# Performance work log

Hardware: AMD Instinct MI355X
Metric: run time of the kernel (lower is better)

Reference implementation:

```python
import jax, jax.numpy as jnp
import numpy as np

N_NODES = 50000
N_EDGES = 800000


def _norm(deg):
    # DGL: norm = deg^-0.5 with inf (zero-degree) replaced by 0
    return jnp.where(deg > 0, jax.lax.rsqrt(jnp.maximum(deg, 1.0)), 0.0)


def setup_inputs() -> dict:
    key = jax.random.key(0)
    ks = jax.random.split(key, 8)
    x = jax.random.normal(ks[0], (N_NODES, 128), dtype=jnp.float32)
    W1 = jax.random.normal(ks[1], (128, 128), dtype=jnp.float32) * (1.0 / np.sqrt(128))
    b1 = jnp.zeros((128,), dtype=jnp.float32)
    W2 = jax.random.normal(ks[2], (128, 8), dtype=jnp.float32) * (1.0 / np.sqrt(128))
    b2 = jnp.zeros((8,), dtype=jnp.float32)
    src = jax.random.randint(ks[3], (N_EDGES,), 0, N_NODES, dtype=jnp.int32)
    dst = jax.random.randint(ks[4], (N_EDGES,), 0, N_NODES, dtype=jnp.int32)
    graph_ids = jnp.sort(jax.random.randint(ks[5], (N_NODES,), 0, 100, dtype=jnp.int32))
    return {"x": x, "W1": W1, "b1": b1, "W2": W2, "b2": b2,
            "src": src, "dst": dst, "graph_ids": graph_ids, "num_graphs": 100}


def _graph_conv(x, W, b, src, dst, norm_src, norm_dst):
    # GraphConv norm='both': out = D_in^{-1/2} A (D_out^{-1/2} x W) + b
    h = x @ W                                   # [N, F_out]
    msg = h[src] * norm_src[src, None]          # gather + src norm, [E, F_out]
    agg = jax.ops.segment_sum(msg, dst, num_segments=x.shape[0])  # scatter-add
    return agg * norm_dst[:, None] + b


def reference(x, W1, b1, W2, b2, src, dst, graph_ids, num_graphs):
    n = x.shape[0]
    ones_e = jnp.ones((src.shape[0],), dtype=x.dtype)
    deg_out = jax.ops.segment_sum(ones_e, src, num_segments=n)
    deg_in = jax.ops.segment_sum(ones_e, dst, num_segments=n)
    norm_src = _norm(deg_out)
    norm_dst = _norm(deg_in)

    h = _graph_conv(x, W1, b1, src, dst, norm_src, norm_dst)
    h = jax.nn.relu(h)
    h = _graph_conv(h, W2, b2, src, dst, norm_src, norm_dst)

    # dgl.mean_nodes: per-graph mean of node features
    counts = jax.ops.segment_sum(jnp.ones((n,), dtype=x.dtype), graph_ids,
                                 num_segments=num_graphs)
    sums = jax.ops.segment_sum(h, graph_ids, num_segments=num_graphs)
    return sums / jnp.maximum(counts, 1.0)[:, None]
```

## Files before the change

### kernel.cpp

```cpp
#include <hip/hip_runtime.h>

#define F1 128
#define F2 8
#define CAP 64
#define RH 8192
#define ECH 16384

typedef unsigned short us8 __attribute__((ext_vector_type(8)));
typedef short b16x8 __attribute__((ext_vector_type(8)));
typedef float f32x4 __attribute__((ext_vector_type(4)));

__device__ inline unsigned short f2bf(float f) {
  unsigned u = __float_as_uint(f);
  u += 0x7FFF + ((u >> 16) & 1);
  return (unsigned short)(u >> 16);
}
__device__ inline float bf2f(unsigned short h) {
  return __uint_as_float(((unsigned)h) << 16);
}

__global__ __launch_bounds__(256) void k_hist(const int* __restrict__ src,
                                              const int* __restrict__ dst,
                                              unsigned short* __restrict__ src16,
                                              unsigned short* __restrict__ dst16,
                                              int* __restrict__ partialA,
                                              int* __restrict__ partialB,
                                              int Epad, int E, int N) {
  __shared__ int binsA[RH];
  __shared__ int binsB[RH];
  int range0 = blockIdx.x * RH;
  int c = blockIdx.y;
  int t = threadIdx.x;
  bool writer = (blockIdx.x == 0);
  for (int i = t; i < RH; i += 256) { binsA[i] = 0; binsB[i] = 0; }
  __syncthreads();
  int e0 = c * ECH, e1 = min(e0 + ECH, Epad);
  for (int base = e0 + t * 4; base < e1; base += 1024) {
    int4 a, b;
    if (base + 4 <= E) {
      a = *(const int4*)&src[base];
      b = *(const int4*)&dst[base];
    } else {
      a.x = (base + 0 < E) ? src[base + 0] : -1;
      a.y = (base + 1 < E) ? src[base + 1] : -1;
      a.z = (base + 2 < E) ? src[base + 2] : -1;
      a.w = (base + 3 < E) ? src[base + 3] : -1;
      b.x = (base + 0 < E) ? dst[base + 0] : -1;
      b.y = (base + 1 < E) ? dst[base + 1] : -1;
      b.z = (base + 2 < E) ? dst[base + 2] : -1;
      b.w = (base + 3 < E) ? dst[base + 3] : -1;
    }
    int av[4] = {a.x, a.y, a.z, a.w};
    int bv[4] = {b.x, b.y, b.z, b.w};
#pragma unroll
    for (int j = 0; j < 4; ++j) {
      int sn = av[j] - range0;
      if (av[j] >= 0 && (unsigned)sn < (unsigned)RH) atomicAdd(&binsA[sn], 1);
      int dn = bv[j] - range0;
      if (bv[j] >= 0 && (unsigned)dn < (unsigned)RH) atomicAdd(&binsB[dn], 1);
    }
    if (writer) {
      ushort4 sa, sb;
      sa.x = av[0] >= 0 ? (unsigned short)av[0] : 0xFFFF;
      sa.y = av[1] >= 0 ? (unsigned short)av[1] : 0xFFFF;
      sa.z = av[2] >= 0 ? (unsigned short)av[2] : 0xFFFF;
      sa.w = av[3] >= 0 ? (unsigned short)av[3] : 0xFFFF;
      sb.x = bv[0] >= 0 ? (unsigned short)bv[0] : 0xFFFF;
      sb.y = bv[1] >= 0 ? (unsigned short)bv[1] : 0xFFFF;
      sb.z = bv[2] >= 0 ? (unsigned short)bv[2] : 0xFFFF;
      sb.w = bv[3] >= 0 ? (unsigned short)bv[3] : 0xFFFF;
      *(ushort4*)&src16[base] = sa;
      *(ushort4*)&dst16[base] = sb;
    }
  }
  __syncthreads();
  for (int i = t; i < RH; i += 256) {
    int n = range0 + i;
    if (n < N) {
      partialA[c * N + n] = binsA[i];
      partialB[c * N + n] = binsB[i];
    }
  }
}

__global__ void k_starts(const int* __restrict__ partialA, const int* __restrict__ partialB,
                         int* __restrict__ starts, int* __restrict__ cnt,
                         float* __restrict__ norm_src, float* __restrict__ norm_dst,
                         unsigned short* __restrict__ esrc16,
                         unsigned short* __restrict__ h1n,
                         float* __restrict__ h2n,
                         float* __restrict__ out,
                         const int* __restrict__ gids,
                         float* __restrict__ rcnt,
                         const float* __restrict__ W1,
                         unsigned short* __restrict__ Wth,
                         unsigned short* __restrict__ Wtl,
                         int N, int NCH, int NG) {
  int n = blockIdx.x * 256 + threadIdx.x;
  if (n < NG * F2) out[n] = 0.f;
  if (n < NG) {
    int g = n;
    int lo = 0, hi = N;
    while (lo < hi) { int m = (lo + hi) >> 1; if (gids[m] < g) lo = m + 1; else hi = m; }
    int lb = lo;
    lo = 0; hi = N;
    while (lo < hi) { int m = (lo + hi) >> 1; if (gids[m] <= g) lo = m + 1; else hi = m; }
    rcnt[g] = 1.f / fmaxf((float)(lo - lb), 1.f);
  }
  if (n < F1 * F1) {
    int k = n >> 7, cc = n & 127;
    float v = W1[n];
    unsigned short hi = f2bf(v);
    unsigned short lo = f2bf(v - bf2f(hi));
    Wth[cc * 128 + k] = hi;
    Wtl[cc * 128 + k] = lo;
  }
  if (n < 16) {
    us8 z = {0, 0, 0, 0, 0, 0, 0, 0};
    *(us8*)&h1n[(size_t)N * 128 + n * 8] = z;
  }
  if (n < 8) h2n[(size_t)N * 8 + n] = 0.f;
  if (n < N) {
    int dout = 0;
#pragma unroll 8
    for (int c = 0; c < NCH; ++c) dout += partialA[c * N + n];
    int run = n * CAP;
#pragma unroll 8
    for (int c = 0; c < NCH; ++c) {
      starts[c * N + n] = run;
      run += partialB[c * N + n];
    }
    int din = run - n * CAP;
    int cn = min(din, CAP);
    cnt[n] = cn;
    int cp = (cn + 15) & ~15;
    for (int pos = cn; pos < cp; ++pos) esrc16[n * CAP + pos] = (unsigned short)N;
    norm_src[n] = dout > 0 ? rsqrtf((float)dout) : 0.f;
    norm_dst[n] = din > 0 ? rsqrtf((float)din) : 0.f;
  }
}

__global__ __launch_bounds__(256) void k_scatter(const unsigned short* __restrict__ src16,
                                                 const unsigned short* __restrict__ dst16,
                                                 const int* __restrict__ starts,
                                                 unsigned short* __restrict__ esrc16,
                                                 int Epad, int N, int NCH) {
  __shared__ int cur[RH];
  int range0 = ((int)blockIdx.x / NCH) * RH;
  int c = (int)blockIdx.x % NCH;
  int t = threadIdx.x;
  for (int i = t; i < RH; i += 256) {
    int n = range0 + i;
    cur[i] = (n < N) ? starts[c * N + n] : 0;
  }
  __syncthreads();
  int e0 = c * ECH, e1 = min(e0 + ECH, Epad);
  for (int base = e0 + t * 8; base < e1; base += 2048) {
    us8 a = *(const us8*)&src16[base];
    us8 b = *(const us8*)&dst16[base];
#pragma unroll
    for (int j = 0; j < 8; ++j) {
      int dn = (int)b[j] - range0;
      if ((unsigned)dn < (unsigned)RH) {
        int node = range0 + dn;
        int p = atomicAdd(&cur[dn], 1);
        if (p < (node + 1) * CAP) esrc16[p] = a[j];
      }
    }
  }
}

__global__ __launch_bounds__(256) void k_gemm1(const float* __restrict__ x,
                                               const unsigned short* __restrict__ Wth,
                                               const unsigned short* __restrict__ Wtl,
                                               const float* __restrict__ norm_src,
                                               unsigned short* __restrict__ h1n, int N) {
  __shared__ unsigned short xh[64][72], xl[64][72];
  __shared__ unsigned short wh[128][72], wl[128][72];
  int tid = threadIdx.x;
  int row0 = blockIdx.x * 64;
  int L = tid & 63;
  int wave = tid >> 6;
  int q = L >> 4, mloc = L & 15;
  int m0 = wave * 16;
  f32x4 acc[8];
#pragma unroll
  for (int t = 0; t < 8; ++t) acc[t] = (f32x4){0.f, 0.f, 0.f, 0.f};

  for (int kb = 0; kb < 2; ++kb) {
    __syncthreads();
#pragma unroll
    for (int it = 0; it < 4; ++it) {
      int flat = tid + it * 256;
      int n = flat >> 3, kg = (flat & 7) * 8;
      us8 vh = *(const us8*)&Wth[n * 128 + kb * 64 + kg];
      us8 vl = *(const us8*)&Wtl[n * 128 + kb * 64 + kg];
      *(us8*)&wh[n][kg] = vh;
      *(us8*)&wl[n][kg] = vl;
    }
#pragma unroll
    for (int it = 0; it < 4; ++it) {
      int idx = tid + it * 256;
      int r = idx >> 4, kk = (idx & 15) * 4;
      int grow = row0 + r;
      float4 v = make_float4(0.f, 0.f, 0.f, 0.f);
      if (grow < N) v = *(const float4*)&x[(size_t)grow * 128 + kb * 64 + kk];
      ushort4 h, l;
      h.x = f2bf(v.x); l.x = f2bf(v.x - bf2f(h.x));
      h.y = f2bf(v.y); l.y = f2bf(v.y - bf2f(h.y));
      h.z = f2bf(v.z); l.z = f2bf(v.z - bf2f(h.z));
      h.w = f2bf(v.w); l.w = f2bf(v.w - bf2f(h.w));
      *(ushort4*)&xh[r][kk] = h;
      *(ushort4*)&xl[r][kk] = l;
    }
    __syncthreads();
#pragma unroll
    for (int ks = 0; ks < 2; ++ks) {
      int koff = ks * 32 + q * 8;
      b16x8 ah = *(const b16x8*)&xh[m0 + mloc][koff];
      b16x8 al = *(const b16x8*)&xl[m0 + mloc][koff];
#pragma unroll
      for (int t = 0; t < 8; ++t) {
        b16x8 bh = *(const b16x8*)&wh[t * 16 + mloc][koff];
        b16x8 bl = *(const b16x8*)&wl[t * 16 + mloc][koff];
        acc[t] = __builtin_amdgcn_mfma_f32_16x16x32_bf16(ah, bh, acc[t], 0, 0, 0);
        acc[t] = __builtin_amdgcn_mfma_f32_16x16x32_bf16(ah, bl, acc[t], 0, 0, 0);
        acc[t] = __builtin_amdgcn_mfma_f32_16x16x32_bf16(al, bh, acc[t], 0, 0, 0);
      }
    }
  }
  int rows[4];
  float ns[4];
#pragma unroll
  for (int reg = 0; reg < 4; ++reg) {
    rows[reg] = row0 + m0 + q * 4 + reg;
    ns[reg] = (rows[reg] < N) ? norm_src[rows[reg]] : 0.f;
  }
#pragma unroll
  for (int t = 0; t < 8; ++t) {
    int col = t * 16 + mloc;
#pragma unroll
    for (int reg = 0; reg < 4; ++reg) {
      if (rows[reg] < N)
        h1n[(size_t)rows[reg] * 128 + col] = f2bf(acc[t][reg] * ns[reg]);
    }
  }
}

__global__ __launch_bounds__(256) void k_aggA(const unsigned short* __restrict__ h1n,
                                              const int* __restrict__ cnt,
                                              const unsigned short* __restrict__ esrc16,
                                              const float* __restrict__ norm_dst,
                                              const float* __restrict__ b1,
                                              float* __restrict__ h1b,
                                              int N, int NB) {
  int tid = threadIdx.x;
  int fc = (int)blockIdx.x / NB;
  int b  = (int)blockIdx.x % NB;
  int lane = tid & 63;
  int wave = tid >> 6;
  int nloc = lane >> 2;
  int sl = lane & 3;
  int node = b * 64 + wave * 16 + nloc;
  if (node >= N) return;
  int cp = (cnt[node] + 15) & ~15;
  int fb = fc * 32 + sl * 8;
  size_t i0 = (size_t)node * CAP;
  float acc[8] = {0.f, 0.f, 0.f, 0.f, 0.f, 0.f, 0.f, 0.f};
  for (int i = 0; i < cp; i += 16) {
#pragma unroll
    for (int h = 0; h < 16; h += 8) {
      ushort4 sA = *(const ushort4*)&esrc16[i0 + i + h];
      ushort4 sB = *(const ushort4*)&esrc16[i0 + i + h + 4];
      us8 v0 = *(const us8*)&h1n[(size_t)sA.x * 128 + fb];
      us8 v1 = *(const us8*)&h1n[(size_t)sA.y * 128 + fb];
      us8 v2 = *(const us8*)&h1n[(size_t)sA.z * 128 + fb];
      us8 v3 = *(const us8*)&h1n[(size_t)sA.w * 128 + fb];
      us8 v4 = *(const us8*)&h1n[(size_t)sB.x * 128 + fb];
      us8 v5 = *(const us8*)&h1n[(size_t)sB.y * 128 + fb];
      us8 v6 = *(const us8*)&h1n[(size_t)sB.z * 128 + fb];
      us8 v7 = *(const us8*)&h1n[(size_t)sB.w * 128 + fb];
#pragma unroll
      for (int j = 0; j < 8; ++j)
        acc[j] += ((bf2f(v0[j]) + bf2f(v1[j])) + (bf2f(v2[j]) + bf2f(v3[j]))) +
                  ((bf2f(v4[j]) + bf2f(v5[j])) + (bf2f(v6[j]) + bf2f(v7[j])));
    }
  }
  float nd = norm_dst[node];
  float4 bb0 = *(const float4*)&b1[fb];
  float4 bb1 = *(const float4*)&b1[fb + 4];
  float4 o0, o1;
  o0.x = fmaxf(acc[0] * nd + bb0.x, 0.f);
  o0.y = fmaxf(acc[1] * nd + bb0.y, 0.f);
  o0.z = fmaxf(acc[2] * nd + bb0.z, 0.f);
  o0.w = fmaxf(acc[3] * nd + bb0.w, 0.f);
  o1.x = fmaxf(acc[4] * nd + bb1.x, 0.f);
  o1.y = fmaxf(acc[5] * nd + bb1.y, 0.f);
  o1.z = fmaxf(acc[6] * nd + bb1.z, 0.f);
  o1.w = fmaxf(acc[7] * nd + bb1.w, 0.f);
  *(float4*)&h1b[(size_t)node * 128 + fb] = o0;
  *(float4*)&h1b[(size_t)node * 128 + fb + 4] = o1;
}

__global__ __launch_bounds__(256) void k_aggB(const float* __restrict__ h1b,
                                              const float* __restrict__ W2,
                                              const float* __restrict__ norm_src,
                                              float* __restrict__ h2n, int N) {
  __shared__ float W2l[128 * 8];
  int tid = threadIdx.x;
  for (int i = tid; i < 1024; i += 256) W2l[i] = W2[i];
  __syncthreads();
  int g = blockIdx.x * 256 + tid;
  int node = g >> 3, j = g & 7;
  if (node >= N) return;
  const float* row = h1b + (size_t)node * 128;
  float acc = 0.f;
#pragma unroll
  for (int k = 0; k < 128; k += 4) {
    float4 v = *(const float4*)&row[k];
    acc += v.x * W2l[(k + 0) * 8 + j] + v.y * W2l[(k + 1) * 8 + j] +
           v.z * W2l[(k + 2) * 8 + j] + v.w * W2l[(k + 3) * 8 + j];
  }
  h2n[g] = acc * norm_src[node];
}

__global__ __launch_bounds__(256) void k_agg2pool(const float* __restrict__ h2n,
                                                  const int* __restrict__ cnt,
                                                  const unsigned short* __restrict__ esrc16,
                                                  const float* __restrict__ norm_dst,
                                                  const float* __restrict__ b2,
                                                  const int* __restrict__ gids,
                                                  const float* __restrict__ rcnt,
                                                  float* __restrict__ out, int N) {
  __shared__ float bins[16 * 8];
  __shared__ int sg0;
  int tid = threadIdx.x;
  if (tid < 128) bins[tid] = 0.f;
  int base = blockIdx.x * 32;
  if (tid == 0) sg0 = gids[min(base, N - 1)];
  __syncthreads();
  int node = base + (tid >> 3);
  int j = tid & 7;
  if (node < N) {
    int cp = (cnt[node] + 15) & ~15;
    int i0 = node * CAP;
    float acc = 0.f;
    for (int i = 0; i < cp; i += 8) {
      us8 ss = *(const us8*)&esrc16[i0 + i];
      acc += ((h2n[(size_t)ss[0] * 8 + j] + h2n[(size_t)ss[1] * 8 + j]) +
              (h2n[(size_t)ss[2] * 8 + j] + h2n[(size_t)ss[3] * 8 + j])) +
             ((h2n[(size_t)ss[4] * 8 + j] + h2n[(size_t)ss[5] * 8 + j]) +
              (h2n[(size_t)ss[6] * 8 + j] + h2n[(size_t)ss[7] * 8 + j]));
    }
    float r = acc * norm_dst[node] + b2[j];
    int gid = gids[node];
    int delta = gid - sg0;
    if (delta < 16) atomicAdd(&bins[delta * 8 + j], r);
    else atomicAdd(&out[gid * 8 + j], r * rcnt[gid]);
  }
  __syncthreads();
  if (tid < 128) {
    float v = bins[tid];
    if (v != 0.f) {
      int gq = sg0 + (tid >> 3);
      atomicAdd(&out[gq * 8 + (tid & 7)], v * rcnt[gq]);
    }
  }
}

extern "C" void kernel_launch(void* const* d_in, const int* in_sizes, int n_in,
                              void* d_out, int out_size, void* d_ws, size_t ws_size,
                              hipStream_t stream) {
  const float* x  = (const float*)d_in[0];
  const float* W1 = (const float*)d_in[1];
  const float* b1 = (const float*)d_in[2];
  const float* W2 = (const float*)d_in[3];
  const float* b2 = (const float*)d_in[4];
  const int* src  = (const int*)d_in[5];
  const int* dst  = (const int*)d_in[6];
  const int* gids = (const int*)d_in[7];
  int N = in_sizes[0] / F1;
  int E = in_sizes[5];
  int NG = out_size / F2;
  float* out = (float*)d_out;

  int Epad = (E + 2047) & ~2047;
  int NR  = (N + RH - 1) / RH;
  int NCH = (Epad + ECH - 1) / ECH;
  int NB  = (N + 63) / 64;

  char* p = (char*)d_ws;
  auto alloc = [&](size_t bytes) -> void* {
    void* r = (void*)p;
    p += (bytes + 255) & ~(size_t)255;
    return r;
  };
  float* rcnt    = (float*)alloc((size_t)NG * 4);
  unsigned short* src16 = (unsigned short*)alloc((size_t)Epad * 2);
  unsigned short* dst16 = (unsigned short*)alloc((size_t)Epad * 2);
  int* cnt       = (int*)alloc((size_t)N * 4);
  float* norm_src = (float*)alloc((size_t)N * 4);
  float* norm_dst = (float*)alloc((size_t)N * 4);
  unsigned short* esrc16 = (unsigned short*)alloc((size_t)N * CAP * 2);
  unsigned short* h1n = (unsigned short*)alloc((size_t)(N + 1) * F1 * 2);
  float* h1b     = (float*)alloc((size_t)N * F1 * 4);
  float* h2n     = (float*)alloc((size_t)(N + 1) * F2 * 4);
  unsigned short* Wth = (unsigned short*)alloc((size_t)F1 * F1 * 2);
  unsigned short* Wtl = (unsigned short*)alloc((size_t)F1 * F1 * 2);
  int* partialA  = (int*)alloc((size_t)NCH * N * 4);
  int* partialB  = (int*)alloc((size_t)NCH * N * 4);
  int* starts    = (int*)alloc((size_t)NCH * N * 4);
  (void)ws_size; (void)n_in;

  k_hist<<<dim3(NR, NCH), 256, 0, stream>>>(src, dst, src16, dst16,
                                            partialA, partialB, Epad, E, N);
  k_starts<<<(N + 255) / 256, 256, 0, stream>>>(partialA, partialB, starts, cnt,
                                                norm_src, norm_dst, esrc16, h1n, h2n,
                                                out, gids, rcnt, W1, Wth, Wtl, N, NCH, NG);
  k_scatter<<<NR * NCH, 256, 0, stream>>>(src16, dst16, starts, esrc16, Epad, N, NCH);
  k_gemm1<<<(N + 63) / 64, 256, 0, stream>>>(x, Wth, Wtl, norm_src, h1n, N);
  k_aggA<<<4 * NB, 256, 0, stream>>>(h1n, cnt, esrc16, norm_dst, b1, h1b, N, NB);
  k_aggB<<<((size_t)N * 8 + 255) / 256, 256, 0, stream>>>(h1b, W2, norm_src, h2n, N);
  k_agg2pool<<<((N * 8 + 255) / 256), 256, 0, stream>>>(h2n, cnt, esrc16, norm_dst, b2,
                                                        gids, rcnt, out, N);
}
```

Before: 219.1 us.

## Split histogram by src/dst, store hidden layer as bf16, vectorize pooled aggregation

The histogram kernel now gives src and dst their own blocks through a third grid dimension, using one larger shared bin array instead of two. The intermediate hidden activations after ReLU are stored as bf16 instead of fp32, which halves the write and read traffic between the aggregation and the second projection. The final aggregate-and-pool kernel has each thread handle two output features with float2 loads, which halves the thread count. Storing bf16 adds rounding error to the layer-1 output.

```diff
diff --git a/kernel.cpp b/kernel.cpp
--- a/kernel.cpp
+++ b/kernel.cpp
@@ -3,7 +3,7 @@
 #define F1 128
 #define F2 8
 #define CAP 64
-#define RH 8192
+#define RH 16384
 #define ECH 16384
 
 typedef unsigned short us8 __attribute__((ext_vector_type(8)));
@@ -26,60 +26,47 @@
                                               int* __restrict__ partialA,
                                               int* __restrict__ partialB,
                                               int Epad, int E, int N) {
-  __shared__ int binsA[RH];
-  __shared__ int binsB[RH];
+  __shared__ int bins[RH];
   int range0 = blockIdx.x * RH;
   int c = blockIdx.y;
+  int which = blockIdx.z;
+  const int* idxp = which ? dst : src;
+  int* partial = which ? partialB : partialA;
+  unsigned short* out16 = which ? dst16 : src16;
   int t = threadIdx.x;
   bool writer = (blockIdx.x == 0);
-  for (int i = t; i < RH; i += 256) { binsA[i] = 0; binsB[i] = 0; }
+  for (int i = t; i < RH; i += 256) bins[i] = 0;
   __syncthreads();
   int e0 = c * ECH, e1 = min(e0 + ECH, Epad);
   for (int base = e0 + t * 4; base < e1; base += 1024) {
-    int4 a, b;
+    int4 a;
     if (base + 4 <= E) {
-      a = *(const int4*)&src[base];
-      b = *(const int4*)&dst[base];
+      a = *(const int4*)&idxp[base];
     } else {
-      a.x = (base + 0 < E) ? src[base + 0] : -1;
-      a.y = (base + 1 < E) ? src[base + 1] : -1;
-      a.z = (base + 2 < E) ? src[base + 2] : -1;
-      a.w = (base + 3 < E) ? src[base + 3] : -1;
-      b.x = (base + 0 < E) ? dst[base + 0] : -1;
-      b.y = (base + 1 < E) ? dst[base + 1] : -1;
-      b.z = (base + 2 < E) ? dst[base + 2] : -1;
-      b.w = (base + 3 < E) ? dst[base + 3] : -1;
+      a.x = (base + 0 < E) ? idxp[base + 0] : -1;
+      a.y = (base + 1 < E) ? idxp[base + 1] : -1;
+      a.z = (base + 2 < E) ? idxp[base + 2] : -1;
+      a.w = (base + 3 < E) ? idxp[base + 3] : -1;
     }
     int av[4] = {a.x, a.y, a.z, a.w};
-    int bv[4] = {b.x, b.y, b.z, b.w};
 #pragma unroll
     for (int j = 0; j < 4; ++j) {
       int sn = av[j] - range0;
-      if (av[j] >= 0 && (unsigned)sn < (unsigned)RH) atomicAdd(&binsA[sn], 1);
-      int dn = bv[j] - range0;
-      if (bv[j] >= 0 && (unsigned)dn < (unsigned)RH) atomicAdd(&binsB[dn], 1);
+      if (av[j] >= 0 && (unsigned)sn < (unsigned)RH) atomicAdd(&bins[sn], 1);
     }
     if (writer) {
-      ushort4 sa, sb;
+      ushort4 sa;
       sa.x = av[0] >= 0 ? (unsigned short)av[0] : 0xFFFF;
       sa.y = av[1] >= 0 ? (unsigned short)av[1] : 0xFFFF;
       sa.z = av[2] >= 0 ? (unsigned short)av[2] : 0xFFFF;
       sa.w = av[3] >= 0 ? (unsigned short)av[3] : 0xFFFF;
-      sb.x = bv[0] >= 0 ? (unsigned short)bv[0] : 0xFFFF;
-      sb.y = bv[1] >= 0 ? (unsigned short)bv[1] : 0xFFFF;
-      sb.z = bv[2] >= 0 ? (unsigned short)bv[2] : 0xFFFF;
-      sb.w = bv[3] >= 0 ? (unsigned short)bv[3] : 0xFFFF;
-      *(ushort4*)&src16[base] = sa;
-      *(ushort4*)&dst16[base] = sb;
+      *(ushort4*)&out16[base] = sa;
     }
   }
   __syncthreads();
   for (int i = t; i < RH; i += 256) {
     int n = range0 + i;
-    if (n < N) {
-      partialA[c * N + n] = binsA[i];
-      partialB[c * N + n] = binsB[i];
-    }
+    if (n < N) partial[c * N + n] = bins[i];
   }
 }
 
@@ -252,7 +239,7 @@
                                               const unsigned short* __restrict__ esrc16,
                                               const float* __restrict__ norm_dst,
                                               const float* __restrict__ b1,
-                                              float* __restrict__ h1b,
+                                              unsigned short* __restrict__ h1b,
                                               int N, int NB) {
   int tid = threadIdx.x;
   int fc = (int)blockIdx.x / NB;
@@ -289,20 +276,19 @@
   float nd = norm_dst[node];
   float4 bb0 = *(const float4*)&b1[fb];
   float4 bb1 = *(const float4*)&b1[fb + 4];
-  float4 o0, o1;
-  o0.x = fmaxf(acc[0] * nd + bb0.x, 0.f);
-  o0.y = fmaxf(acc[1] * nd + bb0.y, 0.f);
-  o0.z = fmaxf(acc[2] * nd + bb0.z, 0.f);
-  o0.w = fmaxf(acc[3] * nd + bb0.w, 0.f);
-  o1.x = fmaxf(acc[4] * nd + bb1.x, 0.f);
-  o1.y = fmaxf(acc[5] * nd + bb1.y, 0.f);
-  o1.z = fmaxf(acc[6] * nd + bb1.z, 0.f);
-  o1.w = fmaxf(acc[7] * nd + bb1.w, 0.f);
-  *(float4*)&h1b[(size_t)node * 128 + fb] = o0;
-  *(float4*)&h1b[(size_t)node * 128 + fb + 4] = o1;
-}
-
-__global__ __launch_bounds__(256) void k_aggB(const float* __restrict__ h1b,
+  us8 o;
+  o[0] = f2bf(fmaxf(acc[0] * nd + bb0.x, 0.f));
+  o[1] = f2bf(fmaxf(acc[1] * nd + bb0.y, 0.f));
+  o[2] = f2bf(fmaxf(acc[2] * nd + bb0.z, 0.f));
+  o[3] = f2bf(fmaxf(acc[3] * nd + bb0.w, 0.f));
+  o[4] = f2bf(fmaxf(acc[4] * nd + bb1.x, 0.f));
+  o[5] = f2bf(fmaxf(acc[5] * nd + bb1.y, 0.f));
+  o[6] = f2bf(fmaxf(acc[6] * nd + bb1.z, 0.f));
+  o[7] = f2bf(fmaxf(acc[7] * nd + bb1.w, 0.f));
+  *(us8*)&h1b[(size_t)node * 128 + fb] = o;
+}
+
+__global__ __launch_bounds__(256) void k_aggB(const unsigned short* __restrict__ h1b,
                                               const float* __restrict__ W2,
                                               const float* __restrict__ norm_src,
                                               float* __restrict__ h2n, int N) {
@@ -313,13 +299,13 @@
   int g = blockIdx.x * 256 + tid;
   int node = g >> 3, j = g & 7;
   if (node >= N) return;
-  const float* row = h1b + (size_t)node * 128;
+  const unsigned short* row = h1b + (size_t)node * 128;
   float acc = 0.f;
 #pragma unroll
-  for (int k = 0; k < 128; k += 4) {
-    float4 v = *(const float4*)&row[k];
-    acc += v.x * W2l[(k + 0) * 8 + j] + v.y * W2l[(k + 1) * 8 + j] +
-           v.z * W2l[(k + 2) * 8 + j] + v.w * W2l[(k + 3) * 8 + j];
+  for (int k = 0; k < 128; k += 8) {
+    us8 v = *(const us8*)&row[k];
+#pragma unroll
+    for (int jj = 0; jj < 8; ++jj) acc += bf2f(v[jj]) * W2l[(k + jj) * 8 + j];
   }
   h2n[g] = acc * norm_src[node];
 }
@@ -336,27 +322,36 @@
   __shared__ int sg0;
   int tid = threadIdx.x;
   if (tid < 128) bins[tid] = 0.f;
-  int base = blockIdx.x * 32;
+  int base = blockIdx.x * 64;
   if (tid == 0) sg0 = gids[min(base, N - 1)];
   __syncthreads();
-  int node = base + (tid >> 3);
-  int j = tid & 7;
+  int node = base + (tid >> 2);
+  int jj = (tid & 3) * 2;
   if (node < N) {
     int cp = (cnt[node] + 15) & ~15;
     int i0 = node * CAP;
-    float acc = 0.f;
+    float2 acc = make_float2(0.f, 0.f);
     for (int i = 0; i < cp; i += 8) {
       us8 ss = *(const us8*)&esrc16[i0 + i];
-      acc += ((h2n[(size_t)ss[0] * 8 + j] + h2n[(size_t)ss[1] * 8 + j]) +
-              (h2n[(size_t)ss[2] * 8 + j] + h2n[(size_t)ss[3] * 8 + j])) +
-             ((h2n[(size_t)ss[4] * 8 + j] + h2n[(size_t)ss[5] * 8 + j]) +
-              (h2n[(size_t)ss[6] * 8 + j] + h2n[(size_t)ss[7] * 8 + j]));
-    }
-    float r = acc * norm_dst[node] + b2[j];
+#pragma unroll
+      for (int e = 0; e < 8; ++e) {
+        float2 v = *(const float2*)&h2n[(size_t)ss[e] * 8 + jj];
+        acc.x += v.x;
+        acc.y += v.y;
+      }
+    }
+    float nd = norm_dst[node];
+    float rx = acc.x * nd + b2[jj];
+    float ry = acc.y * nd + b2[jj + 1];
     int gid = gids[node];
     int delta = gid - sg0;
-    if (delta < 16) atomicAdd(&bins[delta * 8 + j], r);
-    else atomicAdd(&out[gid * 8 + j], r * rcnt[gid]);
+    if (delta < 16) {
+      atomicAdd(&bins[delta * 8 + jj], rx);
+      atomicAdd(&bins[delta * 8 + jj + 1], ry);
+    } else {
+      atomicAdd(&out[gid * 8 + jj], rx * rcnt[gid]);
+      atomicAdd(&out[gid * 8 + jj + 1], ry * rcnt[gid]);
+    }
   }
   __syncthreads();
   if (tid < 128) {
@@ -403,7 +398,7 @@
   float* norm_dst = (float*)alloc((size_t)N * 4);
   unsigned short* esrc16 = (unsigned short*)alloc((size_t)N * CAP * 2);
   unsigned short* h1n = (unsigned short*)alloc((size_t)(N + 1) * F1 * 2);
-  float* h1b     = (float*)alloc((size_t)N * F1 * 4);
+  unsigned short* h1b = (unsigned short*)alloc((size_t)N * F1 * 2);
   float* h2n     = (float*)alloc((size_t)(N + 1) * F2 * 4);
   unsigned short* Wth = (unsigned short*)alloc((size_t)F1 * F1 * 2);
   unsigned short* Wtl = (unsigned short*)alloc((size_t)F1 * F1 * 2);
@@ -412,8 +407,8 @@
   int* starts    = (int*)alloc((size_t)NCH * N * 4);
   (void)ws_size; (void)n_in;
 
-  k_hist<<<dim3(NR, NCH), 256, 0, stream>>>(src, dst, src16, dst16,
-                                            partialA, partialB, Epad, E, N);
+  k_hist<<<dim3(NR, NCH, 2), 256, 0, stream>>>(src, dst, src16, dst16,
+                                               partialA, partialB, Epad, E, N);
   k_starts<<<(N + 255) / 256, 256, 0, stream>>>(partialA, partialB, starts, cnt,
                                                 norm_src, norm_dst, esrc16, h1n, h2n,
                                                 out, gids, rcnt, W1, Wth, Wtl, N, NCH, NG);
@@ -421,6 +416,6 @@
   k_gemm1<<<(N + 63) / 64, 256, 0, stream>>>(x, Wth, Wtl, norm_src, h1n, N);
   k_aggA<<<4 * NB, 256, 0, stream>>>(h1n, cnt, esrc16, norm_dst, b1, h1b, N, NB);
   k_aggB<<<((size_t)N * 8 + 255) / 256, 256, 0, stream>>>(h1b, W2, norm_src, h2n, N);
-  k_agg2pool<<<((N * 8 + 255) / 256), 256, 0, stream>>>(h2n, cnt, esrc16, norm_dst, b2,
+  k_agg2pool<<<((N * 4 + 255) / 256), 256, 0, stream>>>(h2n, cnt, esrc16, norm_dst, b2,
                                                         gids, rcnt, out, N);
 }
```

New measurement: 223.9 us. +2.2%, slower.
